# Optimization experiments

Hardware: AMD Instinct MI355X
Metric: run time of the kernel (lower is better)

Reference implementation:

```python
import jax, jax.numpy as jnp
import numpy as np

B, H, W, C = 2, 256, 256, 192
HEADS, WIN, SHIFT = 6, 8, 4
HID = 4 * C
N = WIN * WIN            # tokens per window
HD = C // HEADS
SCALE = HD ** -0.5

# ---- static relative-position index (matches torch buffer construction) ----
_c = np.stack(np.meshgrid(np.arange(WIN), np.arange(WIN), indexing='ij')).reshape(2, -1)
_r = (_c[:, :, None] - _c[:, None, :]).transpose(1, 2, 0)
_r[..., 0] += WIN - 1
_r[..., 1] += WIN - 1
_r[..., 0] *= 2 * WIN - 1
RPI = _r.sum(-1)  # [N, N]

# ---- static shift attention mask (Swin-style region mask, shift_size>0) ----
def _build_shift_mask():
    m = np.zeros((H, W))
    cnt = 0
    sl = (slice(0, -WIN), slice(-WIN, -SHIFT), slice(-SHIFT, None))
    for hs in sl:
        for ws in sl:
            m[hs, ws] = cnt
            cnt += 1
    mw = m.reshape(H // WIN, WIN, W // WIN, WIN).transpose(0, 2, 1, 3).reshape(-1, N)
    am = mw[:, None, :] - mw[:, :, None]  # unsqueeze(1) - unsqueeze(2)
    return jnp.asarray(np.where(am != 0, -100.0, 0.0), jnp.float32)  # [nW, N, N]

ATTN_MASK = _build_shift_mask()

def _win_part(x):  # [B,H,W,c] -> [B*nW, N, c]
    b, c = x.shape[0], x.shape[-1]
    x = x.reshape(b, H // WIN, WIN, W // WIN, WIN, c).transpose(0, 1, 3, 2, 4, 5)
    return x.reshape(-1, N, c)

def _win_rev(w):  # [B*nW, N, c] -> [B,H,W,c]
    c = w.shape[-1]
    x = w.reshape(-1, H // WIN, W // WIN, WIN, WIN, c).transpose(0, 1, 3, 2, 4, 5)
    return x.reshape(-1, H, W, c)

def _ln(x, w, b):
    mu = x.mean(-1, keepdims=True)
    v = ((x - mu) ** 2).mean(-1, keepdims=True)
    return (x - mu) / jnp.sqrt(v + 1e-5) * w + b


def setup_inputs() -> dict:
    key = jax.random.key(0)
    ks = jax.random.split(key, 9)
    s = jnp.float32(0.02)
    f32 = jnp.float32
    return {
        'x': jax.random.normal(ks[0], (B, H * W, C), f32),
        'norm1_w': jnp.ones((C,), f32), 'norm1_b': jnp.zeros((C,), f32),
        'q_w': jax.random.normal(ks[1], (C, C), f32) * s, 'q_b': jnp.zeros((C,), f32),
        'kv_w': jax.random.normal(ks[2], (C, 2 * C), f32) * s, 'kv_b': jnp.zeros((2 * C,), f32),
        'rpb': jax.random.normal(ks[3], ((2 * WIN - 1) ** 2, HEADS), f32) * s,
        'proj_w': jax.random.normal(ks[4], (C, C), f32) * s, 'proj_b': jnp.zeros((C,), f32),
        'norm2_w': jnp.ones((C,), f32), 'norm2_b': jnp.zeros((C,), f32),
        'l1_w': jax.random.normal(ks[5], (C, HID), f32) * s, 'l1_b': jnp.zeros((HID,), f32),
        'dw_w': jax.random.normal(ks[6], (3, 3, 1, HID), f32) * s, 'dw_b': jnp.zeros((HID,), f32),
        'l2_w': jax.random.normal(ks[7], (HID, C), f32) * s, 'l2_b': jnp.zeros((C,), f32),
    }


def reference(x, norm1_w, norm1_b, q_w, q_b, kv_w, kv_b, rpb, proj_w, proj_b,
              norm2_w, norm2_b, l1_w, l1_b, dw_w, dw_b, l2_w, l2_b):
    shortcut = x
    xn = _ln(x, norm1_w, norm1_b)
    q = (xn @ q_w + q_b).reshape(B, H, W, C)
    kv = (xn @ kv_w + kv_b).reshape(B, H, W, 2 * C)
    # cyclic shift
    q = jnp.roll(q, (-SHIFT, -SHIFT), axis=(1, 2))
    kv = jnp.roll(kv, (-SHIFT, -SHIFT), axis=(1, 2))
    # window partition -> heads
    qw = _win_part(q).reshape(-1, N, HEADS, HD).transpose(0, 2, 1, 3)          # [B_,h,N,hd]
    kvw = _win_part(kv).reshape(-1, N, 2, HEADS, HD).transpose(2, 0, 3, 1, 4)
    kw, vw = kvw[0], kvw[1]
    attn = jnp.einsum('bhnd,bhmd->bhnm', qw * SCALE, kw)                       # [B_,h,N,N]
    bias = rpb[RPI.reshape(-1)].reshape(N, N, HEADS).transpose(2, 0, 1)        # [h,N,N]
    attn = attn + bias[None]
    nW = ATTN_MASK.shape[0]
    attn = attn.reshape(B, nW, HEADS, N, N) + ATTN_MASK[None, :, None]
    attn = jax.nn.softmax(attn.reshape(-1, HEADS, N, N), axis=-1)
    y = jnp.einsum('bhnm,bhmd->bnhd', attn, vw).reshape(-1, N, C)
    y = y @ proj_w + proj_b
    xa = _win_rev(y)
    xa = jnp.roll(xa, (SHIFT, SHIFT), axis=(1, 2)).reshape(B, H * W, C)
    x = shortcut + xa
    # LeFF: linear -> GELU -> 3x3 depthwise conv -> GELU -> linear
    xn = _ln(x, norm2_w, norm2_b)
    h = jax.nn.gelu(xn @ l1_w + l1_b, approximate=False).reshape(B, H, W, HID)
    h = jax.lax.conv_general_dilated(h, dw_w, (1, 1), 'SAME',
                                     dimension_numbers=('NHWC', 'HWIO', 'NHWC'),
                                     feature_group_count=HID) + dw_b
    h = jax.nn.gelu(h, approximate=False).reshape(B, H * W, HID)
    return x + (h @ l2_w + l2_b)
```

## Files before the change

### kernel.cpp

```cpp
#include <hip/hip_runtime.h>
#include <math.h>

typedef float f32x4 __attribute__((ext_vector_type(4)));
typedef short bf16x8 __attribute__((ext_vector_type(8)));

__device__ __forceinline__ short f2bf(float f) {
  unsigned u = __builtin_bit_cast(unsigned, f);
  u = (u + 0x7FFFu + ((u >> 16) & 1u)) >> 16;
  return (short)u;
}
__device__ __forceinline__ float bf2f(short s) {
  unsigned u = ((unsigned)(unsigned short)s) << 16;
  return __builtin_bit_cast(float, u);
}
__device__ __forceinline__ float gelu_exact(float x) {
  return 0.5f * x * (1.0f + erff(x * 0.70710678118654752f));
}
__device__ __forceinline__ void gld16(const short* g, short* l) {
  __builtin_amdgcn_global_load_lds(
      (const __attribute__((address_space(1))) void*)g,
      (__attribute__((address_space(3))) void*)l, 16, 0, 0);
}

__device__ __forceinline__ long perm_row(int b, int ho, int wo) {
  int hs = (ho + 252) & 255, ws = (wo + 252) & 255;
  int w = ((hs >> 3) << 5) | (ws >> 3);
  int t = ((hs & 7) << 3) | (ws & 7);
  return ((long)b << 16) | (w << 6) | t;
}
__device__ __forceinline__ long unperm_row(long m) {
  int b = (int)(m >> 16);
  int w = ((int)m >> 6) & 1023, t = (int)m & 63;
  int hs = ((w >> 5) << 3) | (t >> 3);
  int ws = ((w & 31) << 3) | (t & 7);
  int ho = (hs + 4) & 255, wo = (ws + 4) & 255;
  return ((long)b << 16) | (ho << 8) | wo;
}

__global__ __launch_bounds__(256) void ln1_kernel(const float* __restrict__ x,
                                                  const float* __restrict__ w,
                                                  const float* __restrict__ b,
                                                  short* __restrict__ out) {
  int lane = threadIdx.x & 63;
  long row = (long)blockIdx.x * 4 + (threadIdx.x >> 6);
  const float* xr = x + row * 192;
  float v0 = xr[lane], v1 = xr[lane + 64], v2 = xr[lane + 128];
  float s = v0 + v1 + v2, s2 = v0 * v0 + v1 * v1 + v2 * v2;
#pragma unroll
  for (int m = 1; m < 64; m <<= 1) {
    s += __shfl_xor(s, m);
    s2 += __shfl_xor(s2, m);
  }
  float mu = s * (1.0f / 192.0f);
  float rstd = rsqrtf(s2 * (1.0f / 192.0f) - mu * mu + 1e-5f);
  long drow = perm_row((int)(row >> 16), ((int)row >> 8) & 255, (int)row & 255);
  short* o = out + drow * 192;
  o[lane] = f2bf((v0 - mu) * rstd * w[lane] + b[lane]);
  o[lane + 64] = f2bf((v1 - mu) * rstd * w[lane + 64] + b[lane + 64]);
  o[lane + 128] = f2bf((v2 - mu) * rstd * w[lane + 128] + b[lane + 128]);
}

__global__ __launch_bounds__(256) void ln2_kernel(const short* __restrict__ x,
                                                  const float* __restrict__ w,
                                                  const float* __restrict__ b,
                                                  short* __restrict__ out) {
  int lane = threadIdx.x & 63;
  long row = (long)blockIdx.x * 4 + (threadIdx.x >> 6);
  const short* xr = x + row * 192;
  float v0 = bf2f(xr[lane]), v1 = bf2f(xr[lane + 64]), v2 = bf2f(xr[lane + 128]);
  float s = v0 + v1 + v2, s2 = v0 * v0 + v1 * v1 + v2 * v2;
#pragma unroll
  for (int m = 1; m < 64; m <<= 1) {
    s += __shfl_xor(s, m);
    s2 += __shfl_xor(s2, m);
  }
  float mu = s * (1.0f / 192.0f);
  float rstd = rsqrtf(s2 * (1.0f / 192.0f) - mu * mu + 1e-5f);
  short* o = out + row * 192;
  o[lane] = f2bf((v0 - mu) * rstd * w[lane] + b[lane]);
  o[lane + 64] = f2bf((v1 - mu) * rstd * w[lane + 64] + b[lane + 64]);
  o[lane + 128] = f2bf((v2 - mu) * rstd * w[lane + 128] + b[lane + 128]);
}

__global__ __launch_bounds__(256) void wprep_kernel(const float* __restrict__ w,
                                                    short* __restrict__ bt,
                                                    int K, int N) {
  long i = (long)blockIdx.x * 256 + threadIdx.x;
  if (i >= (long)K * N) return;
  int n = (int)(i / K), k = (int)(i % K);
  bt[i] = f2bf(w[(long)k * N + n]);
}

__global__ __launch_bounds__(256) void bias_prep(const float* __restrict__ rpb,
                                                 float* __restrict__ biasTab) {
  int i = blockIdx.x * 256 + threadIdx.x;
  int k = i & 63, q = (i >> 6) & 63, h = i >> 12;
  int dr = (q >> 3) - (k >> 3) + 7;
  int dc = (q & 7) - (k & 7) + 7;
  biasTab[i] = rpb[(dr * 15 + dc) * 6 + h] * 1.4426950408889634f;
}

template <int NTOT, int EPI>
__global__ __launch_bounds__(256) void gemm1_kernel(
    const short* __restrict__ A, const short* __restrict__ Bt,
    const float* __restrict__ B0, const float* __restrict__ B1,
    const float* __restrict__ residf, short* __restrict__ outp,
    int nblk, int mgx, int iters, int mtiles) {
  __shared__ short As[128 * 192];
  const int tid = threadIdx.x;
  const int lane = tid & 63, wid = tid >> 6;
  const int lr = lane & 15, lg = lane >> 4;
  const int xcd = blockIdx.x & 7;
  const int i = blockIdx.x >> 3;
  const int n0 = (i % nblk) * 64;
  const int mg = xcd * mgx + i / nblk;

  bf16x8 bf[6][4];
#pragma unroll
  for (int ks = 0; ks < 6; ++ks)
#pragma unroll
    for (int ni = 0; ni < 4; ++ni)
      bf[ks][ni] = *(const bf16x8*)(Bt + (long)(n0 + ni * 16 + lr) * 192 +
                                    ks * 32 + lg * 8);

  int src_s[12];
#pragma unroll
  for (int s = 0; s < 12; ++s) {
    int lo = (wid * 12 + s) * 1024 + lane * 16;
    int r = lo / 384, c = lo % 384;
    src_s[s] = r * 192 + ((c ^ ((r & 7) << 4)) >> 1);
  }
  const int xorv = (lr & 7) << 4;

#pragma unroll 1
  for (int it = 0; it < iters; ++it) {
    int mt = mg * iters + it;
    if (mt >= mtiles) continue;
    long m0 = (long)mt * 128;
    const short* Ab = A + m0 * 192;
    __syncthreads();
#pragma unroll
    for (int s = 0; s < 12; ++s)
      gld16(Ab + src_s[s], As + (wid * 12 + s) * 512);
    __syncthreads();
    f32x4 acc[2][4] = {};
#pragma unroll
    for (int ks = 0; ks < 6; ++ks) {
      const char* asb = (const char*)As;
      const int col = (ks * 64 + lg * 16) ^ xorv;
      bf16x8 a0 = *(const bf16x8*)(asb + (wid * 32 + lr) * 384 + col);
      bf16x8 a1 = *(const bf16x8*)(asb + (wid * 32 + 16 + lr) * 384 + col);
#pragma unroll
      for (int ni = 0; ni < 4; ++ni) {
        acc[0][ni] = __builtin_amdgcn_mfma_f32_16x16x32_bf16(a0, bf[ks][ni],
                                                             acc[0][ni], 0, 0, 0);
        acc[1][ni] = __builtin_amdgcn_mfma_f32_16x16x32_bf16(a1, bf[ks][ni],
                                                             acc[1][ni], 0, 0, 0);
      }
    }
#pragma unroll
    for (int mi = 0; mi < 2; ++mi) {
#pragma unroll
      for (int ni = 0; ni < 4; ++ni) {
        int n = n0 + ni * 16 + lr;
        long rowb = m0 + wid * 32 + mi * 16 + lg * 4;
#pragma unroll
        for (int r = 0; r < 4; ++r) {
          float v = acc[mi][ni][r];
          long m = rowb + r;
          if constexpr (EPI == 0) {
            float bb = (n < 192) ? B0[n] : B1[n - 192];
            outp[m * NTOT + n] = f2bf(v + bb);
          } else if constexpr (EPI == 2) {
            outp[m * NTOT + n] = f2bf(gelu_exact(v + B0[n]));
          } else {
            long oidx = unperm_row(m) * 192 + n;
            outp[oidx] = f2bf(v + B0[n] + residf[oidx]);
          }
        }
      }
    }
  }
}

__global__ __launch_bounds__(256) void gemm2_kernel(
    const short* __restrict__ A, const short* __restrict__ Bt,
    const float* __restrict__ bias, const short* __restrict__ residb,
    float* __restrict__ outp) {
  __shared__ short As[128][72];
  __shared__ short Bs[192][72];
  const int tid = threadIdx.x;
  const int lane = tid & 63, wid = tid >> 6;
  const int lr = lane & 15, lg = lane >> 4;
  const int wm = wid >> 1, wn = wid & 1;
  const long m0 = (long)blockIdx.x * 128;

  f32x4 acc[4][6] = {};
#pragma unroll 1
  for (int kc = 0; kc < 12; ++kc) {
    __syncthreads();
#pragma unroll
    for (int p = 0; p < 4; ++p) {
      int g = p * 256 + tid;
      int r = g >> 3, c = g & 7;
      *(float4*)(&As[r][c * 8]) =
          *(const float4*)(A + (m0 + r) * 768 + kc * 64 + c * 8);
    }
#pragma unroll
    for (int p = 0; p < 6; ++p) {
      int g = p * 256 + tid;
      int n = g >> 3, c = g & 7;
      *(float4*)(&Bs[n][c * 8]) =
          *(const float4*)(Bt + (long)n * 768 + kc * 64 + c * 8);
    }
    __syncthreads();
#pragma unroll
    for (int ks = 0; ks < 2; ++ks) {
      bf16x8 a[4], b[6];
#pragma unroll
      for (int mf = 0; mf < 4; ++mf)
        a[mf] = *(const bf16x8*)(&As[wm * 64 + mf * 16 + lr][ks * 32 + lg * 8]);
#pragma unroll
      for (int nf = 0; nf < 6; ++nf)
        b[nf] = *(const bf16x8*)(&Bs[wn * 96 + nf * 16 + lr][ks * 32 + lg * 8]);
#pragma unroll
      for (int mf = 0; mf < 4; ++mf)
#pragma unroll
        for (int nf = 0; nf < 6; ++nf)
          acc[mf][nf] = __builtin_amdgcn_mfma_f32_16x16x32_bf16(
              a[mf], b[nf], acc[mf][nf], 0, 0, 0);
    }
  }
#pragma unroll
  for (int mf = 0; mf < 4; ++mf)
#pragma unroll
    for (int nf = 0; nf < 6; ++nf) {
      int n = wn * 96 + nf * 16 + lr;
      long rowb = m0 + wm * 64 + mf * 16 + lg * 4;
#pragma unroll
      for (int r = 0; r < 4; ++r) {
        long idx = (rowb + r) * 192 + n;
        outp[idx] = acc[mf][nf][r] + bias[n] + bf2f(residb[idx]);
      }
    }
}

__global__ __launch_bounds__(64) void attn_kernel(const short* __restrict__ qkv,
                                                  const float* __restrict__ biasTab,
                                                  short* __restrict__ y) {
  __shared__ short vT[32][72];
  __shared__ short P[64][72];
  const int lane = threadIdx.x;
  const int bid = blockIdx.x;
  const int xcd = bid & 7;
  const int j = bid >> 3;
  const int wglob = xcd * 256 + j / 6;
  const int h = j % 6;
  const int w = wglob & 1023;
  const int wr = w >> 5, wc = w & 31;
  const long wbase = (long)wglob * 64;
  const int lr = lane & 15, lg = lane >> 4;

  bf16x8 aq[4], bk[4];
#pragma unroll
  for (int i = 0; i < 4; ++i) {
    long rq = wbase + i * 16 + lr;
    aq[i] = *(const bf16x8*)(qkv + rq * 576 + h * 32 + lg * 8);
    bk[i] = *(const bf16x8*)(qkv + rq * 576 + 192 + h * 32 + lg * 8);
  }
  {
    const short* vp = qkv + (wbase + lane) * 576 + 384 + h * 32;
#pragma unroll
    for (int q4 = 0; q4 < 4; ++q4) {
      bf16x8 vv = *(const bf16x8*)(vp + q4 * 8);
#pragma unroll
      for (int jj = 0; jj < 8; ++jj) vT[q4 * 8 + jj][lane] = vv[jj];
    }
  }

  f32x4 s[4][4] = {};
#pragma unroll
  for (int mi = 0; mi < 4; ++mi)
#pragma unroll
    for (int ni = 0; ni < 4; ++ni)
      s[mi][ni] = __builtin_amdgcn_mfma_f32_16x16x32_bf16(aq[mi], bk[ni],
                                                          s[mi][ni], 0, 0, 0);

  const float SCL2 = 0.17677669529663687f * 1.4426950408889634f;
  const float MASKC = -144.26950408889634f;
  const bool edge = (wr == 31) || (wc == 31);
  int ridk[4] = {0, 0, 0, 0};
  if (edge) {
#pragma unroll
    for (int ni = 0; ni < 4; ++ni) {
      int k = ni * 16 + lr;
      int kh = wr * 8 + (k >> 3), kw = wc * 8 + (k & 7);
      ridk[ni] = 3 * ((kh < 248) ? 0 : ((kh < 252) ? 1 : 2)) +
                 ((kw < 248) ? 0 : ((kw < 252) ? 1 : 2));
    }
  }

  float rinv[4][4];
#pragma unroll
  for (int mi = 0; mi < 4; ++mi) {
#pragma unroll
    for (int r = 0; r < 4; ++r) {
      int q = mi * 16 + lg * 4 + r;
      const float* bp = biasTab + (h << 12) + (q << 6);
      int ridq = 0;
      if (edge) {
        int qh = wr * 8 + (q >> 3), qw = wc * 8 + (q & 7);
        ridq = 3 * ((qh < 248) ? 0 : ((qh < 252) ? 1 : 2)) +
               ((qw < 248) ? 0 : ((qw < 252) ? 1 : 2));
      }
      float lv[4];
      float mx = -1e30f;
#pragma unroll
      for (int ni = 0; ni < 4; ++ni) {
        float lvv = s[mi][ni][r] * SCL2 + bp[ni * 16 + lr];
        if (edge && ridq != ridk[ni]) lvv += MASKC;
        lv[ni] = lvv;
        mx = fmaxf(mx, lvv);
      }
#pragma unroll
      for (int m = 1; m < 16; m <<= 1) mx = fmaxf(mx, __shfl_xor(mx, m));
      float sum = 0.0f;
#pragma unroll
      for (int ni = 0; ni < 4; ++ni) {
        float p = exp2f(lv[ni] - mx);
        lv[ni] = p;
        sum += p;
      }
#pragma unroll
      for (int m = 1; m < 16; m <<= 1) sum += __shfl_xor(sum, m);
      rinv[mi][r] = 1.0f / sum;
#pragma unroll
      for (int ni = 0; ni < 4; ++ni) P[q][ni * 16 + lr] = f2bf(lv[ni]);
    }
  }
  __syncthreads();

  f32x4 o[4][2] = {};
#pragma unroll
  for (int ks = 0; ks < 2; ++ks) {
    bf16x8 ap[4], bv[2];
#pragma unroll
    for (int mi = 0; mi < 4; ++mi)
      ap[mi] = *(const bf16x8*)(&P[mi * 16 + lr][ks * 32 + lg * 8]);
#pragma unroll
    for (int ni = 0; ni < 2; ++ni)
      bv[ni] = *(const bf16x8*)(&vT[ni * 16 + lr][ks * 32 + lg * 8]);
#pragma unroll
    for (int mi = 0; mi < 4; ++mi)
#pragma unroll
      for (int ni = 0; ni < 2; ++ni)
        o[mi][ni] = __builtin_amdgcn_mfma_f32_16x16x32_bf16(ap[mi], bv[ni],
                                                            o[mi][ni], 0, 0, 0);
  }
#pragma unroll
  for (int mi = 0; mi < 4; ++mi) {
#pragma unroll
    for (int r = 0; r < 4; ++r) {
      int q = mi * 16 + lg * 4 + r;
      float ri = rinv[mi][r];
#pragma unroll
      for (int ni = 0; ni < 2; ++ni)
        y[(wbase + q) * 192 + h * 32 + ni * 16 + lr] = f2bf(o[mi][ni][r] * ri);
    }
  }
}

__global__ __launch_bounds__(256) void dwconv_kernel(const short* __restrict__ hbc,
                                                     const float* __restrict__ dww,
                                                     const float* __restrict__ dwb,
                                                     short* __restrict__ h2c,
                                                     int yh) {
  int t = blockIdx.x * 256 + threadIdx.x;
  int cg = t % 96;
  int px = t / 96;
  int strip = blockIdx.y;

  float wv[9][8];
#pragma unroll
  for (int tap = 0; tap < 9; ++tap) {
    float4 a = *(const float4*)(dww + tap * 768 + cg * 8);
    float4 b = *(const float4*)(dww + tap * 768 + cg * 8 + 4);
    wv[tap][0] = a.x; wv[tap][1] = a.y; wv[tap][2] = a.z; wv[tap][3] = a.w;
    wv[tap][4] = b.x; wv[tap][5] = b.y; wv[tap][6] = b.z; wv[tap][7] = b.w;
  }
  float bias[8];
  {
    float4 a = *(const float4*)(dwb + cg * 8);
    float4 b = *(const float4*)(dwb + cg * 8 + 4);
    bias[0] = a.x; bias[1] = a.y; bias[2] = a.z; bias[3] = a.w;
    bias[4] = b.x; bias[5] = b.y; bias[6] = b.z; bias[7] = b.w;
  }

#pragma unroll 2
  for (int pp = 0; pp < 16; ++pp) {
    int py = strip * 16 + pp;
    int ybase = yh * 128 + py;
    float acc[8];
#pragma unroll
    for (int j = 0; j < 8; ++j) acc[j] = bias[j];
#pragma unroll
    for (int dy = 0; dy < 3; ++dy) {
      int yy = ybase + dy - 1;
      if (yy < 0 || yy > 255) continue;
      int slot = py + dy;
#pragma unroll
      for (int dx = 0; dx < 3; ++dx) {
        int xx = px + dx - 1;
        if (xx < 0 || xx > 255) continue;
        bf16x8 hv = *(const bf16x8*)(hbc + ((long)slot * 256 + xx) * 768 + cg * 8);
#pragma unroll
        for (int j = 0; j < 8; ++j) acc[j] += bf2f(hv[j]) * wv[dy * 3 + dx][j];
      }
    }
    bf16x8 ov;
#pragma unroll
    for (int j = 0; j < 8; ++j) ov[j] = f2bf(gelu_exact(acc[j]));
    *(bf16x8*)(h2c + ((long)py * 256 + px) * 768 + cg * 8) = ov;
  }
}

extern "C" void kernel_launch(void* const* d_in, const int* in_sizes, int n_in,
                              void* d_out, int out_size, void* d_ws, size_t ws_size,
                              hipStream_t stream) {
  const float* x = (const float*)d_in[0];
  const float* n1w = (const float*)d_in[1];
  const float* n1b = (const float*)d_in[2];
  const float* q_w = (const float*)d_in[3];
  const float* q_b = (const float*)d_in[4];
  const float* kv_w = (const float*)d_in[5];
  const float* kv_b = (const float*)d_in[6];
  const float* rpb = (const float*)d_in[7];
  const float* proj_w = (const float*)d_in[8];
  const float* proj_b = (const float*)d_in[9];
  const float* n2w = (const float*)d_in[10];
  const float* n2b = (const float*)d_in[11];
  const float* l1_w = (const float*)d_in[12];
  const float* l1_b = (const float*)d_in[13];
  const float* dw_w = (const float*)d_in[14];
  const float* dw_b = (const float*)d_in[15];
  const float* l2_w = (const float*)d_in[16];
  const float* l2_b = (const float*)d_in[17];
  float* out = (float*)d_out;

  char* ws = (char*)d_ws;
  short* xn = (short*)ws;
  short* qkv = (short*)(ws + 50331648);
  short* hbc = (short*)(ws + 50331648);
  short* h2c = (short*)(ws + 101449728);
  short* x2bf = (short*)(ws + 201326592);
  short* bt1 = (short*)(ws + 251658240);
  short* bt2 = bt1 + 110592;
  short* bt3 = bt2 + 36864;
  short* bt4 = bt3 + 147456;
  float* biasTab = (float*)(ws + 252542976);
  short* yb = xn;
  short* xn2 = xn;

  wprep_kernel<<<144, 256, 0, stream>>>(q_w, bt1, 192, 192);
  wprep_kernel<<<288, 256, 0, stream>>>(kv_w, bt1 + 36864, 192, 384);
  wprep_kernel<<<144, 256, 0, stream>>>(proj_w, bt2, 192, 192);
  wprep_kernel<<<576, 256, 0, stream>>>(l1_w, bt3, 192, 768);
  wprep_kernel<<<576, 256, 0, stream>>>(l2_w, bt4, 768, 192);
  bias_prep<<<96, 256, 0, stream>>>(rpb, biasTab);

  ln1_kernel<<<32768, 256, 0, stream>>>(x, n1w, n1b, xn);
  gemm1_kernel<576, 0><<<1152, 256, 0, stream>>>(xn, bt1, q_b, kv_b, nullptr,
                                                 qkv, 9, 16, 8, 1024);
  attn_kernel<<<12288, 64, 0, stream>>>(qkv, biasTab, yb);
  gemm1_kernel<192, 3><<<384, 256, 0, stream>>>(yb, bt2, proj_b, nullptr, x,
                                                x2bf, 3, 16, 8, 1024);
  ln2_kernel<<<32768, 256, 0, stream>>>(x2bf, n2w, n2b, xn2);

  for (int c = 0; c < 4; ++c) {
    int b = c >> 1, yh = c & 1;
    int ystart = yh ? 127 : 0;
    int s0 = yh ? 0 : 1;
    long tok0 = (long)b * 65536 + (long)ystart * 256;
    long ooff = ((long)b * 65536 + (long)yh * 32768) * 192;
    gemm1_kernel<768, 2><<<864, 256, 0, stream>>>(
        xn2 + tok0 * 192, bt3, l1_b, nullptr, nullptr,
        hbc + (long)s0 * 196608, 12, 9, 4, 258);
    dwconv_kernel<<<dim3(96, 8), 256, 0, stream>>>(hbc, dw_w, dw_b, h2c, yh);
    gemm2_kernel<<<256, 256, 0, stream>>>(h2c, bt4, l2_b, x2bf + ooff,
                                          out + ooff);
  }
}
```

Before: 787.0 us.

## Fuse QKV projection, window attention and output projection into one kernel

Replaces the QKV GEMM, the per-head attention kernel and the projection GEMM with one kernel, launched once per window with 384 threads (six waves, one per head). Q, K and V, the probabilities and the attention output stay in about 107 KB of shared memory, so the 576-wide QKV tensor and the attention output are no longer written to and re-read from global memory. Each block reloads the weight tiles for every window straight from global memory or cache. The large shared-memory footprint limits how many blocks can run at once on a compute unit. The now-unused epilogue variants of gemm1 are removed.

```diff
diff --git a/kernel.cpp b/kernel.cpp
--- a/kernel.cpp
+++ b/kernel.cpp
@@ -100,11 +100,214 @@
   biasTab[i] = rpb[(dr * 15 + dc) * 6 + h] * 1.4426950408889634f;
 }
 
+__global__ __launch_bounds__(384) void fused_attn_kernel(
+    const short* __restrict__ xn, const short* __restrict__ bt1,
+    const short* __restrict__ bt2, const float* __restrict__ q_b,
+    const float* __restrict__ kv_b, const float* __restrict__ proj_b,
+    const float* __restrict__ residf, const float* __restrict__ biasTab,
+    short* __restrict__ x2bf) {
+  __shared__ short S_[54784];
+  const int tid = threadIdx.x;
+  const int lane = tid & 63, wid = tid >> 6;
+  const int lr = lane & 15, lg = lane >> 4;
+  const int bid = blockIdx.x;
+  const int wglob = (bid & 7) * 256 + (bid >> 3);
+  const int w = wglob & 1023;
+  const int wr = w >> 5, wc = w & 31;
+  const long wbase = (long)wglob * 64;
+
+#pragma unroll
+  for (int p = 0; p < 4; ++p) {
+    int g = p * 384 + tid;
+    int r = g / 24, c = g % 24;
+    *(float4*)(&S_[r * 232 + c * 8]) =
+        *(const float4*)(xn + (wbase + r) * 192 + c * 8);
+  }
+  __syncthreads();
+
+  {
+    f32x4 acc[4][6] = {};
+#pragma unroll
+    for (int ks = 0; ks < 6; ++ks) {
+      bf16x8 a[4], bq[6];
+#pragma unroll
+      for (int mf = 0; mf < 4; ++mf)
+        a[mf] = *(const bf16x8*)(&S_[(mf * 16 + lr) * 232 + ks * 32 + lg * 8]);
+#pragma unroll
+      for (int nf = 0; nf < 6; ++nf)
+        bq[nf] = *(const bf16x8*)(bt1 +
+                                  (long)(wid * 96 + nf * 16 + lr) * 192 +
+                                  ks * 32 + lg * 8);
+#pragma unroll
+      for (int mf = 0; mf < 4; ++mf)
+#pragma unroll
+        for (int nf = 0; nf < 6; ++nf)
+          acc[mf][nf] = __builtin_amdgcn_mfma_f32_16x16x32_bf16(
+              a[mf], bq[nf], acc[mf][nf], 0, 0, 0);
+    }
+#pragma unroll
+    for (int mf = 0; mf < 4; ++mf)
+#pragma unroll
+      for (int nf = 0; nf < 6; ++nf) {
+        int col = wid * 96 + nf * 16 + lr;
+#pragma unroll
+        for (int r = 0; r < 4; ++r) {
+          int row = mf * 16 + lg * 4 + r;
+          float v = acc[mf][nf][r];
+          if (wid < 4) {
+            float bb = (wid < 2) ? q_b[col] : kv_b[col - 192];
+            S_[14848 + row * 408 + col] = f2bf(v + bb);
+          } else {
+            int c2 = col - 384;
+            S_[40960 + (c2 >> 5) * 2304 + (c2 & 31) * 72 + row] =
+                f2bf(v + kv_b[c2 + 192]);
+          }
+        }
+      }
+  }
+  __syncthreads();
+
+  const int h = wid;
+  bf16x8 aq[4], bk[4];
+#pragma unroll
+  for (int i = 0; i < 4; ++i) {
+    aq[i] = *(const bf16x8*)(&S_[14848 + (i * 16 + lr) * 408 + h * 32 + lg * 8]);
+    bk[i] = *(const bf16x8*)(&S_[14848 + (i * 16 + lr) * 408 + 192 + h * 32 +
+                                 lg * 8]);
+  }
+  f32x4 s[4][4] = {};
+#pragma unroll
+  for (int mi = 0; mi < 4; ++mi)
+#pragma unroll
+    for (int ni = 0; ni < 4; ++ni)
+      s[mi][ni] = __builtin_amdgcn_mfma_f32_16x16x32_bf16(aq[mi], bk[ni],
+                                                          s[mi][ni], 0, 0, 0);
+  __syncthreads();
+
+  const float SCL2 = 0.17677669529663687f * 1.4426950408889634f;
+  const float MASKC = -144.26950408889634f;
+  const bool edge = (wr == 31) || (wc == 31);
+  int ridk[4] = {0, 0, 0, 0};
+  if (edge) {
+#pragma unroll
+    for (int ni = 0; ni < 4; ++ni) {
+      int k = ni * 16 + lr;
+      int kh = wr * 8 + (k >> 3), kw = wc * 8 + (k & 7);
+      ridk[ni] = 3 * ((kh < 248) ? 0 : ((kh < 252) ? 1 : 2)) +
+                 ((kw < 248) ? 0 : ((kw < 252) ? 1 : 2));
+    }
+  }
+  float rinv[4][4];
+#pragma unroll
+  for (int mi = 0; mi < 4; ++mi) {
+#pragma unroll
+    for (int r = 0; r < 4; ++r) {
+      int q = mi * 16 + lg * 4 + r;
+      const float* bp = biasTab + (h << 12) + (q << 6);
+      int ridq = 0;
+      if (edge) {
+        int qh = wr * 8 + (q >> 3), qw = wc * 8 + (q & 7);
+        ridq = 3 * ((qh < 248) ? 0 : ((qh < 252) ? 1 : 2)) +
+               ((qw < 248) ? 0 : ((qw < 252) ? 1 : 2));
+      }
+      float lv[4];
+      float mx = -1e30f;
+#pragma unroll
+      for (int ni = 0; ni < 4; ++ni) {
+        float lvv = s[mi][ni][r] * SCL2 + bp[ni * 16 + lr];
+        if (edge && ridq != ridk[ni]) lvv += MASKC;
+        lv[ni] = lvv;
+        mx = fmaxf(mx, lvv);
+      }
+#pragma unroll
+      for (int m = 1; m < 16; m <<= 1) mx = fmaxf(mx, __shfl_xor(mx, m));
+      float sum = 0.0f;
+#pragma unroll
+      for (int ni = 0; ni < 4; ++ni) {
+        float p = exp2f(lv[ni] - mx);
+        lv[ni] = p;
+        sum += p;
+      }
+#pragma unroll
+      for (int m = 1; m < 16; m <<= 1) sum += __shfl_xor(sum, m);
+      rinv[mi][r] = 1.0f / sum;
+#pragma unroll
+      for (int ni = 0; ni < 4; ++ni)
+        S_[h * 4608 + q * 72 + ni * 16 + lr] = f2bf(lv[ni]);
+    }
+  }
+
+  f32x4 o[4][2] = {};
+#pragma unroll
+  for (int ks = 0; ks < 2; ++ks) {
+    bf16x8 ap[4], bv[2];
+#pragma unroll
+    for (int mi = 0; mi < 4; ++mi)
+      ap[mi] = *(const bf16x8*)(&S_[h * 4608 + (mi * 16 + lr) * 72 + ks * 32 +
+                                    lg * 8]);
+#pragma unroll
+    for (int ni = 0; ni < 2; ++ni)
+      bv[ni] = *(const bf16x8*)(&S_[40960 + h * 2304 + (ni * 16 + lr) * 72 +
+                                    ks * 32 + lg * 8]);
+#pragma unroll
+    for (int mi = 0; mi < 4; ++mi)
+#pragma unroll
+      for (int ni = 0; ni < 2; ++ni)
+        o[mi][ni] = __builtin_amdgcn_mfma_f32_16x16x32_bf16(ap[mi], bv[ni],
+                                                            o[mi][ni], 0, 0, 0);
+  }
+#pragma unroll
+  for (int mi = 0; mi < 4; ++mi)
+#pragma unroll
+    for (int r = 0; r < 4; ++r) {
+      int q = mi * 16 + lg * 4 + r;
+      float ri = rinv[mi][r];
+#pragma unroll
+      for (int ni = 0; ni < 2; ++ni)
+        S_[27648 + q * 200 + h * 32 + ni * 16 + lr] = f2bf(o[mi][ni][r] * ri);
+    }
+  __syncthreads();
+
+  {
+    f32x4 acc[4][2] = {};
+#pragma unroll
+    for (int ks = 0; ks < 6; ++ks) {
+      bf16x8 a[4], bq[2];
+#pragma unroll
+      for (int mf = 0; mf < 4; ++mf)
+        a[mf] = *(const bf16x8*)(&S_[27648 + (mf * 16 + lr) * 200 + ks * 32 +
+                                     lg * 8]);
+#pragma unroll
+      for (int nf = 0; nf < 2; ++nf)
+        bq[nf] = *(const bf16x8*)(bt2 +
+                                  (long)(wid * 32 + nf * 16 + lr) * 192 +
+                                  ks * 32 + lg * 8);
+#pragma unroll
+      for (int mf = 0; mf < 4; ++mf)
+#pragma unroll
+        for (int nf = 0; nf < 2; ++nf)
+          acc[mf][nf] = __builtin_amdgcn_mfma_f32_16x16x32_bf16(
+              a[mf], bq[nf], acc[mf][nf], 0, 0, 0);
+    }
+#pragma unroll
+    for (int mf = 0; mf < 4; ++mf)
+#pragma unroll
+      for (int nf = 0; nf < 2; ++nf) {
+        int n = wid * 32 + nf * 16 + lr;
+#pragma unroll
+        for (int r = 0; r < 4; ++r) {
+          long m = wbase + mf * 16 + lg * 4 + r;
+          long oidx = unperm_row(m) * 192 + n;
+          x2bf[oidx] = f2bf(acc[mf][nf][r] + proj_b[n] + residf[oidx]);
+        }
+      }
+  }
+}
+
 template <int NTOT, int EPI>
 __global__ __launch_bounds__(256) void gemm1_kernel(
     const short* __restrict__ A, const short* __restrict__ Bt,
-    const float* __restrict__ B0, const float* __restrict__ B1,
-    const float* __restrict__ residf, short* __restrict__ outp,
+    const float* __restrict__ B0, short* __restrict__ outp,
     int nblk, int mgx, int iters, int mtiles) {
   __shared__ short As[128 * 192];
   const int tid = threadIdx.x;
@@ -166,17 +369,8 @@
         long rowb = m0 + wid * 32 + mi * 16 + lg * 4;
 #pragma unroll
         for (int r = 0; r < 4; ++r) {
-          float v = acc[mi][ni][r];
           long m = rowb + r;
-          if constexpr (EPI == 0) {
-            float bb = (n < 192) ? B0[n] : B1[n - 192];
-            outp[m * NTOT + n] = f2bf(v + bb);
-          } else if constexpr (EPI == 2) {
-            outp[m * NTOT + n] = f2bf(gelu_exact(v + B0[n]));
-          } else {
-            long oidx = unperm_row(m) * 192 + n;
-            outp[oidx] = f2bf(v + B0[n] + residf[oidx]);
-          }
+          outp[m * NTOT + n] = f2bf(gelu_exact(acc[mi][ni][r] + B0[n]));
         }
       }
     }
@@ -243,131 +437,6 @@
         outp[idx] = acc[mf][nf][r] + bias[n] + bf2f(residb[idx]);
       }
     }
-}
-
-__global__ __launch_bounds__(64) void attn_kernel(const short* __restrict__ qkv,
-                                                  const float* __restrict__ biasTab,
-                                                  short* __restrict__ y) {
-  __shared__ short vT[32][72];
-  __shared__ short P[64][72];
-  const int lane = threadIdx.x;
-  const int bid = blockIdx.x;
-  const int xcd = bid & 7;
-  const int j = bid >> 3;
-  const int wglob = xcd * 256 + j / 6;
-  const int h = j % 6;
-  const int w = wglob & 1023;
-  const int wr = w >> 5, wc = w & 31;
-  const long wbase = (long)wglob * 64;
-  const int lr = lane & 15, lg = lane >> 4;
-
-  bf16x8 aq[4], bk[4];
-#pragma unroll
-  for (int i = 0; i < 4; ++i) {
-    long rq = wbase + i * 16 + lr;
-    aq[i] = *(const bf16x8*)(qkv + rq * 576 + h * 32 + lg * 8);
-    bk[i] = *(const bf16x8*)(qkv + rq * 576 + 192 + h * 32 + lg * 8);
-  }
-  {
-    const short* vp = qkv + (wbase + lane) * 576 + 384 + h * 32;
-#pragma unroll
-    for (int q4 = 0; q4 < 4; ++q4) {
-      bf16x8 vv = *(const bf16x8*)(vp + q4 * 8);
-#pragma unroll
-      for (int jj = 0; jj < 8; ++jj) vT[q4 * 8 + jj][lane] = vv[jj];
-    }
-  }
-
-  f32x4 s[4][4] = {};
-#pragma unroll
-  for (int mi = 0; mi < 4; ++mi)
-#pragma unroll
-    for (int ni = 0; ni < 4; ++ni)
-      s[mi][ni] = __builtin_amdgcn_mfma_f32_16x16x32_bf16(aq[mi], bk[ni],
-                                                          s[mi][ni], 0, 0, 0);
-
-  const float SCL2 = 0.17677669529663687f * 1.4426950408889634f;
-  const float MASKC = -144.26950408889634f;
-  const bool edge = (wr == 31) || (wc == 31);
-  int ridk[4] = {0, 0, 0, 0};
-  if (edge) {
-#pragma unroll
-    for (int ni = 0; ni < 4; ++ni) {
-      int k = ni * 16 + lr;
-      int kh = wr * 8 + (k >> 3), kw = wc * 8 + (k & 7);
-      ridk[ni] = 3 * ((kh < 248) ? 0 : ((kh < 252) ? 1 : 2)) +
-                 ((kw < 248) ? 0 : ((kw < 252) ? 1 : 2));
-    }
-  }
-
-  float rinv[4][4];
-#pragma unroll
-  for (int mi = 0; mi < 4; ++mi) {
-#pragma unroll
-    for (int r = 0; r < 4; ++r) {
-      int q = mi * 16 + lg * 4 + r;
-      const float* bp = biasTab + (h << 12) + (q << 6);
-      int ridq = 0;
-      if (edge) {
-        int qh = wr * 8 + (q >> 3), qw = wc * 8 + (q & 7);
-        ridq = 3 * ((qh < 248) ? 0 : ((qh < 252) ? 1 : 2)) +
-               ((qw < 248) ? 0 : ((qw < 252) ? 1 : 2));
-      }
-      float lv[4];
-      float mx = -1e30f;
-#pragma unroll
-      for (int ni = 0; ni < 4; ++ni) {
-        float lvv = s[mi][ni][r] * SCL2 + bp[ni * 16 + lr];
-        if (edge && ridq != ridk[ni]) lvv += MASKC;
-        lv[ni] = lvv;
-        mx = fmaxf(mx, lvv);
-      }
-#pragma unroll
-      for (int m = 1; m < 16; m <<= 1) mx = fmaxf(mx, __shfl_xor(mx, m));
-      float sum = 0.0f;
-#pragma unroll
-      for (int ni = 0; ni < 4; ++ni) {
-        float p = exp2f(lv[ni] - mx);
-        lv[ni] = p;
-        sum += p;
-      }
-#pragma unroll
-      for (int m = 1; m < 16; m <<= 1) sum += __shfl_xor(sum, m);
-      rinv[mi][r] = 1.0f / sum;
-#pragma unroll
-      for (int ni = 0; ni < 4; ++ni) P[q][ni * 16 + lr] = f2bf(lv[ni]);
-    }
-  }
-  __syncthreads();
-
-  f32x4 o[4][2] = {};
-#pragma unroll
-  for (int ks = 0; ks < 2; ++ks) {
-    bf16x8 ap[4], bv[2];
-#pragma unroll
-    for (int mi = 0; mi < 4; ++mi)
-      ap[mi] = *(const bf16x8*)(&P[mi * 16 + lr][ks * 32 + lg * 8]);
-#pragma unroll
-    for (int ni = 0; ni < 2; ++ni)
-      bv[ni] = *(const bf16x8*)(&vT[ni * 16 + lr][ks * 32 + lg * 8]);
-#pragma unroll
-    for (int mi = 0; mi < 4; ++mi)
-#pragma unroll
-      for (int ni = 0; ni < 2; ++ni)
-        o[mi][ni] = __builtin_amdgcn_mfma_f32_16x16x32_bf16(ap[mi], bv[ni],
-                                                            o[mi][ni], 0, 0, 0);
-  }
-#pragma unroll
-  for (int mi = 0; mi < 4; ++mi) {
-#pragma unroll
-    for (int r = 0; r < 4; ++r) {
-      int q = mi * 16 + lg * 4 + r;
-      float ri = rinv[mi][r];
-#pragma unroll
-      for (int ni = 0; ni < 2; ++ni)
-        y[(wbase + q) * 192 + h * 32 + ni * 16 + lr] = f2bf(o[mi][ni][r] * ri);
-    }
-  }
 }
 
 __global__ __launch_bounds__(256) void dwconv_kernel(const short* __restrict__ hbc,
@@ -449,7 +518,6 @@
 
   char* ws = (char*)d_ws;
   short* xn = (short*)ws;
-  short* qkv = (short*)(ws + 50331648);
   short* hbc = (short*)(ws + 50331648);
   short* h2c = (short*)(ws + 101449728);
   short* x2bf = (short*)(ws + 201326592);
@@ -458,7 +526,6 @@
   short* bt3 = bt2 + 36864;
   short* bt4 = bt3 + 147456;
   float* biasTab = (float*)(ws + 252542976);
-  short* yb = xn;
   short* xn2 = xn;
 
   wprep_kernel<<<144, 256, 0, stream>>>(q_w, bt1, 192, 192);
@@ -469,11 +536,8 @@
   bias_prep<<<96, 256, 0, stream>>>(rpb, biasTab);
 
   ln1_kernel<<<32768, 256, 0, stream>>>(x, n1w, n1b, xn);
-  gemm1_kernel<576, 0><<<1152, 256, 0, stream>>>(xn, bt1, q_b, kv_b, nullptr,
-                                                 qkv, 9, 16, 8, 1024);
-  attn_kernel<<<12288, 64, 0, stream>>>(qkv, biasTab, yb);
-  gemm1_kernel<192, 3><<<384, 256, 0, stream>>>(yb, bt2, proj_b, nullptr, x,
-                                                x2bf, 3, 16, 8, 1024);
+  fused_attn_kernel<<<2048, 384, 0, stream>>>(xn, bt1, bt2, q_b, kv_b, proj_b,
+                                              x, biasTab, x2bf);
   ln2_kernel<<<32768, 256, 0, stream>>>(x2bf, n2w, n2b, xn2);
 
   for (int c = 0; c < 4; ++c) {
@@ -483,8 +547,7 @@
     long tok0 = (long)b * 65536 + (long)ystart * 256;
     long ooff = ((long)b * 65536 + (long)yh * 32768) * 192;
     gemm1_kernel<768, 2><<<864, 256, 0, stream>>>(
-        xn2 + tok0 * 192, bt3, l1_b, nullptr, nullptr,
-        hbc + (long)s0 * 196608, 12, 9, 4, 258);
+        xn2 + tok0 * 192, bt3, l1_b, hbc + (long)s0 * 196608, 12, 9, 4, 258);
     dwconv_kernel<<<dim3(96, 8), 256, 0, stream>>>(hbc, dw_w, dw_b, h2c, yh);
     gemm2_kernel<<<256, 256, 0, stream>>>(h2c, bt4, l2_b, x2bf + ooff,
                                           out + ooff);
```

Result: slower. 840.4 us (+6.8%).
